# Optimization experiments

Hardware: AMD Instinct MI355X
Metric: run time of the kernel (lower is better)

Reference implementation:

```python
import jax, jax.numpy as jnp
import numpy as np

B, S, H = 4, 4096, 2048
NH, HD = 16, 128
DFF = 8192
CAPACITY = 0.5
EPS = 1e-5


def setup_inputs() -> dict:
    key = jax.random.key(0)
    ks = jax.random.split(key, 11)
    s_h = 1.0 / np.sqrt(H)
    s_f = 1.0 / np.sqrt(DFF)
    return {
        "hidden_states": jax.random.normal(ks[0], (B, S, H), jnp.float32),
        "w_router": jax.random.normal(ks[1], (H,), jnp.float32) * s_h,
        "b_router": jnp.zeros((1,), jnp.float32),
        "Wq": jax.random.normal(ks[2], (H, H), jnp.float32) * s_h,
        "Wk": jax.random.normal(ks[3], (H, H), jnp.float32) * s_h,
        "Wv": jax.random.normal(ks[4], (H, H), jnp.float32) * s_h,
        "Wo": jax.random.normal(ks[5], (H, H), jnp.float32) * s_h,
        "w_gate": jax.random.normal(ks[6], (H, DFF), jnp.float32) * s_h,
        "w_up": jax.random.normal(ks[7], (H, DFF), jnp.float32) * s_h,
        "w_down": jax.random.normal(ks[8], (DFF, H), jnp.float32) * s_f,
        "norm1_w": jnp.ones((H,), jnp.float32),
        "norm2_w": jnp.ones((H,), jnp.float32),
    }


def _rmsnorm(x, w):
    var = jnp.mean(jnp.square(x), axis=-1, keepdims=True)
    return x * jax.lax.rsqrt(var + EPS) * w


def reference(hidden_states, w_router, b_router, Wq, Wk, Wv, Wo,
              w_gate, w_up, w_down, norm1_w, norm2_w):
    x = hidden_states  # [B,S,H]
    # --- router: sigmoid(Wx+b), select top-k per row, ties via >= threshold ---
    logits = jnp.einsum("bsh,h->bs", x, w_router) + b_router[0]
    weights = jax.nn.sigmoid(logits)  # [B,S]
    k = max(1, int(CAPACITY * S))
    topk_vals, _ = jax.lax.top_k(weights, k)
    threshold = topk_vals[:, -1:]
    mask = weights >= threshold  # [B,S] bool

    # --- full block, computed per-token (attention is over seq_len==1) ---
    n1 = _rmsnorm(x, norm1_w)
    q = (n1 @ Wq).reshape(B, S, NH, HD)
    kk = (n1 @ Wk).reshape(B, S, NH, HD)
    v = (n1 @ Wv).reshape(B, S, NH, HD)
    # each selected token is its own length-1 sequence -> softmax over 1 pos == 1
    scores = jnp.einsum("bshd,bshd->bsh", q, kk) / np.sqrt(HD)
    attn_w = jax.nn.softmax(scores[..., None], axis=-1)  # [B,S,NH,1], all ones
    ctx = (attn_w * v).reshape(B, S, H)
    attn_out = ctx @ Wo

    res = x + attn_out
    n2 = _rmsnorm(res, norm2_w)
    ffn = (jax.nn.silu(n2 @ w_gate) * (n2 @ w_up)) @ w_down
    out_full = res + ffn

    # scatter back: non-selected tokens pass through unchanged
    out = jnp.where(mask[..., None], out_full, x)
    return out
```

## Files before the change

kernel.cpp:

```cpp
#include <hip/hip_runtime.h>
#include <cstdint>
#include <cstddef>

#define B_    4
#define S_    4096
#define H_    2048
#define DFF_  8192
#define KSEL  2048
#define CAP   2304
#define TPB   9
#define TCAP  (B_*CAP)
#define NRT   (TCAP/256)

typedef unsigned short ushort_t;
typedef __attribute__((ext_vector_type(8))) __bf16 bf16x8;
typedef __attribute__((ext_vector_type(4))) float f32x4;

__device__ __forceinline__ ushort_t f2bf(float f) {
  union { float f; uint32_t u; } v; v.f = f;
  uint32_t u = v.u;
  return (ushort_t)((u + 0x7FFFu + ((u >> 16) & 1u)) >> 16);
}
__device__ __forceinline__ float bf2f(ushort_t h) {
  union { uint32_t u; float f; } v; v.u = ((uint32_t)h) << 16;
  return v.f;
}

__device__ __forceinline__ void gload16(const void* g, void* l) {
  __builtin_amdgcn_global_load_lds(
      (const __attribute__((address_space(1))) void*)g,
      (__attribute__((address_space(3))) void*)l, 16, 0, 0);
}

#define SBAR()                                  \
  do {                                          \
    asm volatile("" ::: "memory");              \
    __builtin_amdgcn_s_barrier();               \
    asm volatile("" ::: "memory");              \
  } while (0)

__global__ __launch_bounds__(256) void wconvT_k(const float* __restrict__ W,
                                                ushort_t* __restrict__ Wt,
                                                int K, int N) {
  __shared__ float tile[64][65];
  int k0 = blockIdx.x * 64, n0 = blockIdx.y * 64;
  int tx = threadIdx.x & 63, ty = threadIdx.x >> 6;
  #pragma unroll
  for (int yy = ty; yy < 64; yy += 4)
    tile[yy][tx] = W[(size_t)(k0 + yy) * N + n0 + tx];
  __syncthreads();
  #pragma unroll
  for (int yy = ty; yy < 64; yy += 4)
    Wt[(size_t)(n0 + yy) * K + k0 + tx] = f2bf(tile[tx][yy]);
}

__global__ __launch_bounds__(256) void router_k(const float* __restrict__ x,
                                                const float* __restrict__ wr,
                                                const float* __restrict__ br,
                                                float* __restrict__ wts) {
  int t = blockIdx.x * 4 + (threadIdx.x >> 6);
  int lane = threadIdx.x & 63;
  const float4* xr = (const float4*)(x + (size_t)t * H_);
  const float4* w4 = (const float4*)wr;
  float s = 0.f;
  #pragma unroll
  for (int j = 0; j < 8; ++j) {
    float4 a = xr[lane + 64 * j], b = w4[lane + 64 * j];
    s = fmaf(a.x, b.x, s); s = fmaf(a.y, b.y, s);
    s = fmaf(a.z, b.z, s); s = fmaf(a.w, b.w, s);
  }
  #pragma unroll
  for (int o = 32; o > 0; o >>= 1) s += __shfl_xor(s, o, 64);
  if (lane == 0) wts[t] = 1.f / (1.f + expf(-(s + br[0])));
}

__global__ __launch_bounds__(1024) void kth_k(const float* __restrict__ wts,
                                              float* __restrict__ thr) {
  __shared__ float a[S_];
  int b = blockIdx.x, tid = threadIdx.x;
  const float* wb = wts + b * S_;
  for (int i = tid; i < S_; i += 1024) a[i] = wb[i];
  for (int size = 2; size <= S_; size <<= 1) {
    for (int stride = size >> 1; stride > 0; stride >>= 1) {
      __syncthreads();
      for (int t = tid; t < S_ / 2; t += 1024) {
        int i = ((t / stride) * (stride << 1)) + (t % stride);
        int j = i + stride;
        bool up = ((i & size) == 0);
        float ai = a[i], aj = a[j];
        if ((ai > aj) == up) { a[i] = aj; a[j] = ai; }
      }
    }
  }
  __syncthreads();
  if (tid == 0) thr[b] = a[S_ - KSEL];
}

__global__ __launch_bounds__(1024) void compact_k(const float* __restrict__ wts,
                                                  const float* __restrict__ thr,
                                                  int* __restrict__ idx,
                                                  int* __restrict__ counts) {
  __shared__ int sc[1024];
  int b = blockIdx.x, tid = threadIdx.x;
  float th = thr[b];
  int m[4], cnt = 0;
  #pragma unroll
  for (int e = 0; e < 4; ++e) {
    m[e] = (wts[b * S_ + tid * 4 + e] >= th) ? 1 : 0;
    cnt += m[e];
  }
  sc[tid] = cnt;
  __syncthreads();
  for (int off = 1; off < 1024; off <<= 1) {
    int add = (tid >= off) ? sc[tid - off] : 0;
    __syncthreads();
    sc[tid] += add;
    __syncthreads();
  }
  int excl = sc[tid] - cnt;
  int total = sc[1023];
  int cl = total < CAP ? total : CAP;
  #pragma unroll
  for (int e = 0; e < 4; ++e) {
    if (m[e]) {
      if (excl < CAP) idx[b * CAP + excl] = b * S_ + tid * 4 + e;
      excl++;
    }
  }
  for (int j2 = tid; j2 < CAP; j2 += 1024)
    if (j2 >= cl) idx[b * CAP + j2] = -1;
  if (tid == 0) counts[b] = cl;
}

template <int MODE>
__global__ __launch_bounds__(256) void rms_k(const float* __restrict__ src,
                                             const float* __restrict__ w,
                                             const int* __restrict__ idx,
                                             const int* __restrict__ counts,
                                             ushort_t* __restrict__ dst) {
  int r = blockIdx.x * 4 + (threadIdx.x >> 6);
  int lane = threadIdx.x & 63;
  ushort4* drow = (ushort4*)(dst + (size_t)r * H_);
  const float* s;
  if (MODE == 0) {
    int b = r / CAP, local = r % CAP;
    if (local >= counts[b]) {
      ushort4 z; z.x = z.y = z.z = z.w = 0;
      #pragma unroll
      for (int j = 0; j < 8; ++j) drow[lane + 64 * j] = z;
      return;
    }
    s = src + (size_t)idx[r] * H_;
  } else {
    s = src + (size_t)r * H_;
  }
  const float4* s4 = (const float4*)s;
  float4 v[8];
  float ss = 0.f;
  #pragma unroll
  for (int j = 0; j < 8; ++j) {
    v[j] = s4[lane + 64 * j];
    ss = fmaf(v[j].x, v[j].x, ss); ss = fmaf(v[j].y, v[j].y, ss);
    ss = fmaf(v[j].z, v[j].z, ss); ss = fmaf(v[j].w, v[j].w, ss);
  }
  #pragma unroll
  for (int o = 32; o > 0; o >>= 1) ss += __shfl_xor(ss, o, 64);
  float rstd = rsqrtf(ss * (1.f / H_) + 1e-5f);
  const float4* w4 = (const float4*)w;
  #pragma unroll
  for (int j = 0; j < 8; ++j) {
    float4 ww = w4[lane + 64 * j];
    ushort4 o4;
    o4.x = f2bf(v[j].x * rstd * ww.x);
    o4.y = f2bf(v[j].y * rstd * ww.y);
    o4.z = f2bf(v[j].z * rstd * ww.z);
    o4.w = f2bf(v[j].w * rstd * ww.w);
    drow[lane + 64 * j] = o4;
  }
}

__global__ void copy_k(const float4* __restrict__ in, float4* __restrict__ out,
                       int n) {
  int i = blockIdx.x * blockDim.x + threadIdx.x;
  int stride = gridDim.x * blockDim.x;
  for (; i < n; i += stride) out[i] = in[i];
}

template <int EPI>
__global__ __launch_bounds__(512, 2) void gemm8_k(
    const ushort_t* __restrict__ A,
    const ushort_t* __restrict__ Bt,
    int K, int N, int nct,
    const int* __restrict__ counts,
    const int* __restrict__ idx,
    const float* __restrict__ xres,
    const ushort_t* __restrict__ gsrc,
    float* __restrict__ outf,
    ushort_t* __restrict__ outh) {
  const int nwg = (int)gridDim.x;
  const int bid = (int)blockIdx.x;
  const int cpx = nwg >> 3;
  const int wg = (bid & 7) * cpx + (bid >> 3);
  const int rt = wg / nct;
  const int ct = wg % nct;
  const int bb = rt / TPB;
  const int local0 = (rt % TPB) << 8;
  if (local0 >= counts[bb]) return;

  extern __shared__ __align__(16) char lds[];

  const int tid = (int)threadIdx.x;
  const int lane = tid & 63;
  const int wave = tid >> 6;
  const int wm = wave >> 2;
  const int wn = wave & 3;

  const int srow = tid >> 3;
  const int schunk = (tid & 7) ^ (srow & 7);
  const size_t Kb = (size_t)K * 2;
  const char* aS = (const char*)A + (size_t)(rt * 256 + srow) * Kb + (size_t)schunk * 16;
  const char* bS = (const char*)Bt + (size_t)(ct * 256 + srow) * Kb + (size_t)schunk * 16;

  const int frow = lane & 15;
  const int fk = lane >> 4;

  f32x4 acc[8][4];
  #pragma unroll
  for (int m = 0; m < 8; ++m)
    #pragma unroll
    for (int n = 0; n < 4; ++n) acc[m][n] = (f32x4){0.f, 0.f, 0.f, 0.f};

  #pragma unroll
  for (int i = 0; i < 4; ++i)
    gload16(aS + (size_t)i * 64 * Kb, lds + i * 8192 + wave * 1024);
  #pragma unroll
  for (int i = 0; i < 4; ++i)
    gload16(bS + (size_t)i * 64 * Kb, lds + 65536 + i * 8192 + wave * 1024);
  asm volatile("s_waitcnt vmcnt(0)" ::: "memory");
  SBAR();

  const int nkt = K >> 6;
  for (int kt = 0; kt < nkt; ++kt) {
    const int po = (kt & 1) << 15;
    const int no = po ^ 32768;
    const char* curA = lds + po;
    const char* curB = lds + 65536 + po;
    char* nxtA = lds + no;
    char* nxtB = lds + 65536 + no;
    const bool pre = (kt + 1 < nkt);
    const size_t kcol = (size_t)(kt + 1) * 128;
    bf16x8 bfr[4][2];

    #pragma unroll
    for (int q = 0; q < 4; ++q) {
      if (q == 0 && pre) {
        #pragma unroll
        for (int i = 0; i < 4; ++i)
          gload16(aS + (size_t)i * 64 * Kb + kcol, nxtA + i * 8192 + wave * 1024);
      }
      if (q == 1 && pre) {
        #pragma unroll
        for (int i = 0; i < 4; ++i)
          gload16(bS + (size_t)i * 64 * Kb + kcol, nxtB + i * 8192 + wave * 1024);
      }
      bf16x8 af[2][2];
      #pragma unroll
      for (int i = 0; i < 2; ++i) {
        const int row = wm * 128 + (2 * q + i) * 16 + frow;
        #pragma unroll
        for (int ks = 0; ks < 2; ++ks)
          af[i][ks] = *(const bf16x8*)(curA + row * 128 +
                                       (((ks * 4 + fk) ^ (row & 7)) << 4));
      }
      if (q == 0) {
        #pragma unroll
        for (int n = 0; n < 4; ++n) {
          const int row = wn * 64 + n * 16 + frow;
          #pragma unroll
          for (int ks = 0; ks < 2; ++ks)
            bfr[n][ks] = *(const bf16x8*)(curB + row * 128 +
                                          (((ks * 4 + fk) ^ (row & 7)) << 4));
        }
      }
      SBAR();
      __builtin_amdgcn_s_setprio(1);
      #pragma unroll
      for (int i = 0; i < 2; ++i)
        #pragma unroll
        for (int ks = 0; ks < 2; ++ks)
          #pragma unroll
          for (int n = 0; n < 4; ++n)
            acc[2 * q + i][n] = __builtin_amdgcn_mfma_f32_16x16x32_bf16(
                af[i][ks], bfr[n][ks], acc[2 * q + i][n], 0, 0, 0);
      __builtin_amdgcn_s_setprio(0);
      if (q == 3) asm volatile("s_waitcnt vmcnt(0)" ::: "memory");
      SBAR();
    }
  }

  const int erow0 = rt * 256 + wm * 128;
  const int ecol0 = ct * 256 + wn * 64;
  const int rq = (lane >> 4) << 2;
  const int cc = lane & 15;
  #pragma unroll
  for (int m = 0; m < 8; ++m) {
    #pragma unroll
    for (int qq = 0; qq < 4; ++qq) {
      const int r = erow0 + m * 16 + rq + qq;
      if (EPI == 0) {
        #pragma unroll
        for (int n = 0; n < 4; ++n)
          outh[(size_t)r * N + ecol0 + n * 16 + cc] = f2bf(acc[m][n][qq]);
      } else if (EPI == 1) {
        const int t = idx[r];
        #pragma unroll
        for (int n = 0; n < 4; ++n) {
          const int c = ecol0 + n * 16 + cc;
          const float xv = (t >= 0) ? xres[(size_t)t * H_ + c] : 0.f;
          outf[(size_t)r * H_ + c] = xv + acc[m][n][qq];
        }
      } else if (EPI == 2) {
        #pragma unroll
        for (int n = 0; n < 4; ++n) {
          const size_t o = (size_t)r * N + ecol0 + n * 16 + cc;
          const float g = bf2f(gsrc[o]);
          const float h = (g / (1.f + expf(-g))) * acc[m][n][qq];
          outh[o] = f2bf(h);
        }
      } else {
        const int t = idx[r];
        if (t >= 0) {
          #pragma unroll
          for (int n = 0; n < 4; ++n) {
            const int c = ecol0 + n * 16 + cc;
            outf[(size_t)t * H_ + c] = xres[(size_t)r * H_ + c] + acc[m][n][qq];
          }
        }
      }
    }
  }
}

extern "C" void kernel_launch(void* const* d_in, const int* in_sizes, int n_in,
                              void* d_out, int out_size, void* d_ws, size_t ws_size,
                              hipStream_t stream) {
  const float* x   = (const float*)d_in[0];
  const float* wr  = (const float*)d_in[1];
  const float* br  = (const float*)d_in[2];
  const float* Wv  = (const float*)d_in[5];
  const float* Wo  = (const float*)d_in[6];
  const float* Wg  = (const float*)d_in[7];
  const float* Wu  = (const float*)d_in[8];
  const float* Wd  = (const float*)d_in[9];
  const float* n1w = (const float*)d_in[10];
  const float* n2w = (const float*)d_in[11];
  float* out = (float*)d_out;

  char* p = (char*)d_ws;
  auto alloc = [&](size_t bytes) {
    char* r = p;
    p += (bytes + 255) & ~(size_t)255;
    return r;
  };
  ushort_t* WvT = (ushort_t*)alloc((size_t)H_ * H_ * 2);
  ushort_t* WoT = (ushort_t*)alloc((size_t)H_ * H_ * 2);
  ushort_t* WgT = (ushort_t*)alloc((size_t)DFF_ * H_ * 2);
  ushort_t* WuT = (ushort_t*)alloc((size_t)DFF_ * H_ * 2);
  ushort_t* WdT = (ushort_t*)alloc((size_t)H_ * DFF_ * 2);
  float* wts    = (float*)alloc((size_t)B_ * S_ * 4);
  float* thr    = (float*)alloc(256);
  int* counts   = (int*)alloc(256);
  int* idx      = (int*)alloc((size_t)TCAP * 4);
  ushort_t* Xn1 = (ushort_t*)alloc((size_t)TCAP * H_ * 2);
  ushort_t* Vc  = (ushort_t*)alloc((size_t)TCAP * H_ * 2);
  float* RES    = (float*)alloc((size_t)TCAP * H_ * 4);
  ushort_t* Hb  = (ushort_t*)alloc((size_t)TCAP * DFF_ * 2);
  (void)ws_size; (void)in_sizes; (void)n_in; (void)out_size;

  wconvT_k<<<dim3(H_ / 64, H_ / 64), 256, 0, stream>>>(Wv, WvT, H_, H_);
  wconvT_k<<<dim3(H_ / 64, H_ / 64), 256, 0, stream>>>(Wo, WoT, H_, H_);
  wconvT_k<<<dim3(H_ / 64, DFF_ / 64), 256, 0, stream>>>(Wg, WgT, H_, DFF_);
  wconvT_k<<<dim3(H_ / 64, DFF_ / 64), 256, 0, stream>>>(Wu, WuT, H_, DFF_);
  wconvT_k<<<dim3(DFF_ / 64, H_ / 64), 256, 0, stream>>>(Wd, WdT, DFF_, H_);

  router_k<<<(B_ * S_) / 4, 256, 0, stream>>>(x, wr, br, wts);
  kth_k<<<B_, 1024, 0, stream>>>(wts, thr);
  compact_k<<<B_, 1024, 0, stream>>>(wts, thr, idx, counts);

  rms_k<0><<<TCAP / 4, 256, 0, stream>>>(x, n1w, idx, counts, Xn1);

  copy_k<<<2048, 256, 0, stream>>>((const float4*)x, (float4*)out,
                                   (B_ * S_ * H_) / 4);

  const size_t LDSB = 131072;
  gemm8_k<0><<<NRT * (H_ / 256), 512, LDSB, stream>>>(
      Xn1, WvT, H_, H_, H_ / 256, counts, idx, nullptr, nullptr, nullptr, Vc);
  gemm8_k<1><<<NRT * (H_ / 256), 512, LDSB, stream>>>(
      Vc, WoT, H_, H_, H_ / 256, counts, idx, x, nullptr, RES, nullptr);
  rms_k<1><<<TCAP / 4, 256, 0, stream>>>(RES, n2w, idx, counts, Xn1);
  gemm8_k<0><<<NRT * (DFF_ / 256), 512, LDSB, stream>>>(
      Xn1, WgT, H_, DFF_, DFF_ / 256, counts, idx, nullptr, nullptr, nullptr, Hb);
  gemm8_k<2><<<NRT * (DFF_ / 256), 512, LDSB, stream>>>(
      Xn1, WuT, H_, DFF_, DFF_ / 256, counts, idx, nullptr, Hb, nullptr, Hb);
  gemm8_k<3><<<NRT * (H_ / 256), 512, LDSB, stream>>>(
      Hb, WdT, DFF_, H_, H_ / 256, counts, idx, RES, nullptr, out, nullptr);
}
```

Before: 1.963 ms.

## Prefetch B tiles two k-steps ahead with split staging and partial vmcnt waits

Restructures the bf16 GEMM main loop into a manually unrolled two-k-tile body. Each A and B tile load is split into halves spread across the four MFMA phases. B is prefetched two tiles ahead, which is possible because its fragments are already in registers after phase 0. The full vmcnt(0) drain becomes vmcnt(4), so the just-issued loads can stay in flight across the barrier. The aim is to hide more global-to-LDS latency behind MFMA work, at the cost of tighter buffer-reuse reasoning and a loop that assumes an even number of k-tiles.

Result: no change. 1.954 ms (-0.5%).

```diff
diff --git a/kernel.cpp b/kernel.cpp
--- a/kernel.cpp
+++ b/kernel.cpp
@@ -38,6 +38,9 @@
     __builtin_amdgcn_s_barrier();               \
     asm volatile("" ::: "memory");              \
   } while (0)
+
+#define VMCNT4 asm volatile("s_waitcnt vmcnt(4)" ::: "memory")
+#define VMCNT0 asm volatile("s_waitcnt vmcnt(0)" ::: "memory")
 
 __global__ __launch_bounds__(256) void wconvT_k(const float* __restrict__ W,
                                                 ushort_t* __restrict__ Wt,
@@ -186,6 +189,39 @@
   for (; i < n; i += stride) out[i] = in[i];
 }
 
+
+#define PHASE(KT, Q, STAGE_STMT, WAIT_STMT)                                    \
+  {                                                                            \
+    const char* curA_ = lds + (((KT) & 1) << 15);                              \
+    const char* curB_ = lds + 65536 + (((KT) & 1) << 15);                      \
+    bf16x8 af[2][2];                                                           \
+    _Pragma("unroll") for (int i_ = 0; i_ < 2; ++i_) {                         \
+      const int row_ = wm * 128 + (2 * (Q) + i_) * 16 + frow;                  \
+      _Pragma("unroll") for (int ks_ = 0; ks_ < 2; ++ks_)                      \
+        af[i_][ks_] = *(const bf16x8*)(curA_ + row_ * 128 +                    \
+                                       (((ks_ * 4 + fk) ^ (row_ & 7)) << 4));  \
+    }                                                                          \
+    if ((Q) == 0) {                                                            \
+      _Pragma("unroll") for (int n_ = 0; n_ < 4; ++n_) {                       \
+        const int row_ = wn * 64 + n_ * 16 + frow;                             \
+        _Pragma("unroll") for (int ks_ = 0; ks_ < 2; ++ks_)                    \
+          bfr[n_][ks_] = *(const bf16x8*)(curB_ + row_ * 128 +                 \
+                                          (((ks_ * 4 + fk) ^ (row_ & 7)) << 4)); \
+      }                                                                        \
+    }                                                                          \
+    STAGE_STMT;                                                                \
+    SBAR();                                                                    \
+    __builtin_amdgcn_s_setprio(1);                                             \
+    _Pragma("unroll") for (int i_ = 0; i_ < 2; ++i_)                           \
+      _Pragma("unroll") for (int ks_ = 0; ks_ < 2; ++ks_)                      \
+        _Pragma("unroll") for (int n_ = 0; n_ < 4; ++n_)                       \
+          acc[2 * (Q) + i_][n_] = __builtin_amdgcn_mfma_f32_16x16x32_bf16(     \
+              af[i_][ks_], bfr[n_][ks_], acc[2 * (Q) + i_][n_], 0, 0, 0);      \
+    __builtin_amdgcn_s_setprio(0);                                             \
+    WAIT_STMT;                                                                 \
+    SBAR();                                                                    \
+  }
+
 template <int EPI>
 __global__ __launch_bounds__(512, 2) void gemm8_k(
     const ushort_t* __restrict__ A,
@@ -224,78 +260,46 @@
   const int frow = lane & 15;
   const int fk = lane >> 4;
 
+  auto stageA = [&](int ktile, int h) {
+    char* dst = lds + ((ktile & 1) << 15);
+    const size_t kcol = (size_t)ktile * 128;
+    #pragma unroll
+    for (int i = 2 * h; i < 2 * h + 2; ++i)
+      gload16(aS + (size_t)i * 64 * Kb + kcol, dst + i * 8192 + wave * 1024);
+  };
+  auto stageB = [&](int ktile, int h) {
+    char* dst = lds + 65536 + ((ktile & 1) << 15);
+    const size_t kcol = (size_t)ktile * 128;
+    #pragma unroll
+    for (int i = 2 * h; i < 2 * h + 2; ++i)
+      gload16(bS + (size_t)i * 64 * Kb + kcol, dst + i * 8192 + wave * 1024);
+  };
+
   f32x4 acc[8][4];
   #pragma unroll
   for (int m = 0; m < 8; ++m)
     #pragma unroll
     for (int n = 0; n < 4; ++n) acc[m][n] = (f32x4){0.f, 0.f, 0.f, 0.f};
 
-  #pragma unroll
-  for (int i = 0; i < 4; ++i)
-    gload16(aS + (size_t)i * 64 * Kb, lds + i * 8192 + wave * 1024);
-  #pragma unroll
-  for (int i = 0; i < 4; ++i)
-    gload16(bS + (size_t)i * 64 * Kb, lds + 65536 + i * 8192 + wave * 1024);
-  asm volatile("s_waitcnt vmcnt(0)" ::: "memory");
+  stageA(0, 0); stageA(0, 1); stageB(0, 0); stageB(0, 1);
+  stageB(1, 0); stageB(1, 1);
+  VMCNT4;
   SBAR();
 
   const int nkt = K >> 6;
-  for (int kt = 0; kt < nkt; ++kt) {
-    const int po = (kt & 1) << 15;
-    const int no = po ^ 32768;
-    const char* curA = lds + po;
-    const char* curB = lds + 65536 + po;
-    char* nxtA = lds + no;
-    char* nxtB = lds + 65536 + no;
-    const bool pre = (kt + 1 < nkt);
-    const size_t kcol = (size_t)(kt + 1) * 128;
+  for (int kt = 0; kt < nkt; kt += 2) {
+    const bool pre = (kt + 2 < nkt);
     bf16x8 bfr[4][2];
-
-    #pragma unroll
-    for (int q = 0; q < 4; ++q) {
-      if (q == 0 && pre) {
-        #pragma unroll
-        for (int i = 0; i < 4; ++i)
-          gload16(aS + (size_t)i * 64 * Kb + kcol, nxtA + i * 8192 + wave * 1024);
-      }
-      if (q == 1 && pre) {
-        #pragma unroll
-        for (int i = 0; i < 4; ++i)
-          gload16(bS + (size_t)i * 64 * Kb + kcol, nxtB + i * 8192 + wave * 1024);
-      }
-      bf16x8 af[2][2];
-      #pragma unroll
-      for (int i = 0; i < 2; ++i) {
-        const int row = wm * 128 + (2 * q + i) * 16 + frow;
-        #pragma unroll
-        for (int ks = 0; ks < 2; ++ks)
-          af[i][ks] = *(const bf16x8*)(curA + row * 128 +
-                                       (((ks * 4 + fk) ^ (row & 7)) << 4));
-      }
-      if (q == 0) {
-        #pragma unroll
-        for (int n = 0; n < 4; ++n) {
-          const int row = wn * 64 + n * 16 + frow;
-          #pragma unroll
-          for (int ks = 0; ks < 2; ++ks)
-            bfr[n][ks] = *(const bf16x8*)(curB + row * 128 +
-                                          (((ks * 4 + fk) ^ (row & 7)) << 4));
-        }
-      }
-      SBAR();
-      __builtin_amdgcn_s_setprio(1);
-      #pragma unroll
-      for (int i = 0; i < 2; ++i)
-        #pragma unroll
-        for (int ks = 0; ks < 2; ++ks)
-          #pragma unroll
-          for (int n = 0; n < 4; ++n)
-            acc[2 * q + i][n] = __builtin_amdgcn_mfma_f32_16x16x32_bf16(
-                af[i][ks], bfr[n][ks], acc[2 * q + i][n], 0, 0, 0);
-      __builtin_amdgcn_s_setprio(0);
-      if (q == 3) asm volatile("s_waitcnt vmcnt(0)" ::: "memory");
-      SBAR();
-    }
+    PHASE(kt, 0, stageA(kt + 1, 0), );
+    PHASE(kt, 1, stageA(kt + 1, 1), );
+    PHASE(kt, 2, if (pre) stageB(kt + 2, 0), );
+    PHASE(kt, 3, if (pre) stageB(kt + 2, 1),
+          if (pre) { VMCNT4; } else { VMCNT0; });
+    PHASE(kt + 1, 0, if (pre) stageA(kt + 2, 0), );
+    PHASE(kt + 1, 1, if (pre) stageA(kt + 2, 1), );
+    PHASE(kt + 1, 2, if (pre) stageB(kt + 3, 0), );
+    PHASE(kt + 1, 3, if (pre) stageB(kt + 3, 1),
+          if (pre) { VMCNT4; } else { VMCNT0; });
   }
 
   const int erow0 = rt * 256 + wm * 128;
```
